# Performance work log

Hardware: AMD Instinct MI355X
Metric: run time of the kernel (lower is better)

## Reference

```python
import jax, jax.numpy as jnp
import numpy as np
from jax import lax

PAD0, PAD1 = 2, 2  # kernel_size=3 -> pad = (3//2+1, (3+1)//2) = (2, 2)


def make_blur_kernel():
    k = jnp.array([1.0, 3.0, 3.0, 1.0], dtype=jnp.float32)
    k2 = k[None, :] * k[:, None]  # [4,4] binomial
    return k2 / jnp.sum(k2)


def setup_inputs() -> dict:
    key = jax.random.key(0)
    x = jax.random.normal(key, (16, 256, 128, 128), dtype=jnp.float32)
    kernel = make_blur_kernel()  # fixed (buffer) 4x4 normalized binomial filter
    return {"x": x, "kernel": kernel}


def reference(x, kernel):
    # upfirdn2d(x, k, up=1, down=1, padding=(2,2)):
    # zero-pad H and W by (2,2) each, depthwise FIR filter with the 4x4 kernel.
    # Kernel is symmetric, so correlation == convolution.
    C = x.shape[1]
    w = jnp.broadcast_to(kernel[None, None, :, :], (C, 1, 4, 4))  # depthwise OIHW
    out = lax.conv_general_dilated(
        x, w,
        window_strides=(1, 1),
        padding=((PAD0, PAD1), (PAD0, PAD1)),
        feature_group_count=C,
        dimension_numbers=("NCHW", "OIHW", "NCHW"),
    )
    # output: [16, 256, 129, 129] (H + pad0 + pad1 - 4 + 1)
    return out
```

## Files before the change

kernel.cpp:

```cpp
#include <hip/hip_runtime.h>


__global__ __launch_bounds__(512) void blur_half3(
    const float* __restrict__ x,
    const float* __restrict__ kern,
    float* __restrict__ out)
{
    __shared__ __align__(16) float lds[69 * 128 + 8 * 264];

    const int tid  = threadIdx.x;
    const int bid  = blockIdx.x;
    const int wk   = ((bid & 7) << 10) | (bid >> 3);
    const int img  = wk >> 1;
    const int s    = wk & 1;
    const int wv   = tid >> 6;
    const int lane = tid & 63;

    const float* __restrict__ xi = x + (size_t)img * (128 * 128);
    float* __restrict__ oi = out + (size_t)img * (129 * 129);

    const int P0 = s ? 0 : 1;
    const int P1 = s ? 32 : 33;
    for (int p = P0 + wv; p <= P1; p += 8) {
        const int row = 64 * s - 2 + 2 * p;
        const float* src = xi + (size_t)row * 128 + (lane << 2);
        const float* dst = &lds[p * 256];
        __builtin_amdgcn_global_load_lds(
            (const __attribute__((address_space(1))) unsigned int*)src,
            (__attribute__((address_space(3))) unsigned int*)dst, 16, 0, 0);
    }
    if (tid < 256) {
        if (s) lds[8448 + tid] = 0.0f;
        else   lds[tid]        = 0.0f;
    } else if (tid < 384) {
        lds[8448 + tid] = 0.0f;
    }

    float w[4][4];
#pragma unroll
    for (int p = 0; p < 4; ++p)
#pragma unroll
        for (int q = 0; q < 4; ++q)
            w[p][q] = kern[4 * p + q];

    __syncthreads();

    const int c  = tid >> 5;
    const int g  = tid & 31;
    const bool lv = (g >= 1);
    const float* const zrow = &lds[68 * 128];
    float* const obuf = &lds[69 * 128 + wv * 264 + (c & 1) * 132];

    float xv[4][8];

#define LLOAD(S, KK) do {                                                    \
        const float* pb_ = &lds[(4 * c + (KK)) * 128 + 4 * g];               \
        const float* pa_ = lv ? (pb_ - 4) : zrow;                            \
        float4 a_ = *(const float4*)pa_;                                     \
        float4 b_ = *(const float4*)pb_;                                     \
        xv[S][0] = a_.x; xv[S][1] = a_.y; xv[S][2] = a_.z; xv[S][3] = a_.w;  \
        xv[S][4] = b_.x; xv[S][5] = b_.y; xv[S][6] = b_.z; xv[S][7] = b_.w;  \
    } while (0)

#define ACCP(S, P) do {                                                      \
        o0 = fmaf(xv[S][0], w[P][0], o0);                                    \
        o1 = fmaf(xv[S][1], w[P][0], o1);                                    \
        o2 = fmaf(xv[S][2], w[P][0], o2);                                    \
        o3 = fmaf(xv[S][3], w[P][0], o3);                                    \
        o0 = fmaf(xv[S][1], w[P][1], o0);                                    \
        o1 = fmaf(xv[S][2], w[P][1], o1);                                    \
        o2 = fmaf(xv[S][3], w[P][1], o2);                                    \
        o3 = fmaf(xv[S][4], w[P][1], o3);                                    \
        o0 = fmaf(xv[S][2], w[P][2], o0);                                    \
        o1 = fmaf(xv[S][3], w[P][2], o1);                                    \
        o2 = fmaf(xv[S][4], w[P][2], o2);                                    \
        o3 = fmaf(xv[S][5], w[P][2], o3);                                    \
        o0 = fmaf(xv[S][3], w[P][3], o0);                                    \
        o1 = fmaf(xv[S][4], w[P][3], o1);                                    \
        o2 = fmaf(xv[S][5], w[P][3], o2);                                    \
        o3 = fmaf(xv[S][6], w[P][3], o3);                                    \
    } while (0)

#define XROW(S, P) do {                                                      \
        e0 = fmaf(xv[S][4], w[P][0], e0);                                    \
        e0 = fmaf(xv[S][5], w[P][1], e0);                                    \
        e0 = fmaf(xv[S][6], w[P][2], e0);                                    \
        e0 = fmaf(xv[S][7], w[P][3], e0);                                    \
        e1 = fmaf(xv[S][5], w[P][0], e1);                                    \
        e1 = fmaf(xv[S][6], w[P][1], e1);                                    \
        e1 = fmaf(xv[S][7], w[P][2], e1);                                    \
        e2 = fmaf(xv[S][6], w[P][0], e2);                                    \
        e2 = fmaf(xv[S][7], w[P][1], e2);                                    \
    } while (0)

#define CS(SA, SB, SC, SD, J) do {                                           \
        float o0 = 0.f, o1 = 0.f, o2 = 0.f, o3 = 0.f;                        \
        ACCP(SA, 0); ACCP(SB, 1); ACCP(SC, 2); ACCP(SD, 3);                  \
        *(float4*)&obuf[4 * g] = make_float4(o0, o1, o2, o3);                \
        if (g == 31) {                                                       \
            float e0 = 0.f, e1 = 0.f, e2 = 0.f;                              \
            XROW(SA, 0); XROW(SB, 1); XROW(SC, 2); XROW(SD, 3);              \
            *(float2*)&obuf[128] = make_float2(e0, e1);    \
            obuf[130] = e2;                                \
        }                                                                    \
        asm volatile("s_waitcnt lgkmcnt(0)" ::: "memory");                   \
        __builtin_amdgcn_sched_barrier(0);                                   \
        {                                                                    \
            float* po_ = oi + (size_t)(64 * s + 4 * c + (J)) * 129;          \
            _Pragma("unroll")                                                \
            for (int k_ = 0; k_ < 4; ++k_)                                   \
                po_[g + 32 * k_] = obuf[2 + g + 32 * k_];                    \
            if (g == 0) po_[128] = obuf[130];                                \
        }                                                                    \
    } while (0)

    {
        LLOAD(0, 0); LLOAD(1, 1); LLOAD(2, 2); LLOAD(3, 3);
        CS(0, 1, 2, 3, 0); LLOAD(0, 4);
        CS(1, 2, 3, 0, 1); LLOAD(1, 5);
        CS(2, 3, 0, 1, 2); LLOAD(2, 6);
        CS(3, 0, 1, 2, 3);
        if (s == 1 && c == 15) {
            LLOAD(3, 7);
            CS(0, 1, 2, 3, 4);
        }
    }

#undef LLOAD
#undef ACCP
#undef XROW
#undef CS
}

extern "C" void kernel_launch(void* const* d_in, const int* in_sizes, int n_in,
                              void* d_out, int out_size, void* d_ws, size_t ws_size,
                              hipStream_t stream) {
    const float* x    = (const float*)d_in[0];
    const float* kern = (const float*)d_in[1];
    float* out        = (float*)d_out;

    dim3 grid(8192), block(512);
    hipLaunchKernelGGL(blur_half3, grid, block, 0, stream, x, kern, out);
}
```

Measured before the change: 109.9 us.

## Replace block barrier with producer-consumer LDS flag pipeline and direct stores

Wave 0 now issues all global-to-LDS row loads and publishes progress through an LDS flag as vmcnt drains, while the other waves spin on the flag and start computing as soon as their rows land. This replaces the full __syncthreads after loading. The LDS staging buffer for output rows is removed, and results are written straight to global memory with unaligned scalar stores. Out-of-range rows are clamped on load and masked to zero when read. The risks are spin-wait overhead, a single wave issuing all the loads, poorer store coalescing, and depending on LDS flag ordering being correct.

```diff
diff --git a/kernel.cpp b/kernel.cpp
--- a/kernel.cpp
+++ b/kernel.cpp
@@ -1,12 +1,12 @@
 #include <hip/hip_runtime.h>
 
 
-__global__ __launch_bounds__(512) void blur_half3(
+__global__ __launch_bounds__(512) void blur_pc(
     const float* __restrict__ x,
     const float* __restrict__ kern,
     float* __restrict__ out)
 {
-    __shared__ __align__(16) float lds[69 * 128 + 8 * 264];
+    __shared__ __align__(16) float lds[68 * 128 + 128 + 4];
 
     const int tid  = threadIdx.x;
     const int bid  = blockIdx.x;
@@ -15,49 +15,64 @@
     const int s    = wk & 1;
     const int wv   = tid >> 6;
     const int lane = tid & 63;
+    const int h    = lane >> 5;
+    const int g    = lane & 31;
+    const bool lv  = (g >= 1);
 
-    const float* __restrict__ xi = x + (size_t)img * (128 * 128);
-    float* __restrict__ oi = out + (size_t)img * (129 * 129);
+    const float* __restrict__ xi = x + (size_t)img * 16384;
+    float* __restrict__ oi = out + (size_t)img * 16641;
 
-    const int P0 = s ? 0 : 1;
-    const int P1 = s ? 32 : 33;
-    for (int p = P0 + wv; p <= P1; p += 8) {
-        const int row = 64 * s - 2 + 2 * p;
-        const float* src = xi + (size_t)row * 128 + (lane << 2);
-        const float* dst = &lds[p * 256];
-        __builtin_amdgcn_global_load_lds(
-            (const __attribute__((address_space(1))) unsigned int*)src,
-            (__attribute__((address_space(3))) unsigned int*)dst, 16, 0, 0);
-    }
-    if (tid < 256) {
-        if (s) lds[8448 + tid] = 0.0f;
-        else   lds[tid]        = 0.0f;
-    } else if (tid < 384) {
-        lds[8448 + tid] = 0.0f;
-    }
+    volatile int* flag = (volatile int*)&lds[68 * 128 + 128];
+    const float* const zrow = &lds[68 * 128];
 
     float w[4][4];
 #pragma unroll
     for (int p = 0; p < 4; ++p)
 #pragma unroll
-        for (int q = 0; q < 4; ++q)
-            w[p][q] = kern[4 * p + q];
+        for (int d = 0; d < 4; ++d)
+            w[p][d] = kern[4 * p + d];
+    __builtin_amdgcn_sched_barrier(0);
 
-    __syncthreads();
+    if (tid < 128) lds[68 * 128 + tid] = 0.0f;
+    if (tid == 0)  *flag = 0;
+    asm volatile("s_waitcnt lgkmcnt(0)" ::: "memory");
+    __builtin_amdgcn_s_barrier();
 
-    const int c  = tid >> 5;
-    const int g  = tid & 31;
-    const bool lv = (g >= 1);
-    const float* const zrow = &lds[68 * 128];
-    float* const obuf = &lds[69 * 128 + wv * 264 + (c & 1) * 132];
+    if (wv == 0) {
+        for (int p = 0; p < 34; ++p) {
+            int row = 64 * s - 2 + 2 * p;
+            row = row < 0 ? 0 : (row > 126 ? 126 : row);
+            const float* src = xi + (size_t)row * 128 + (lane << 2);
+            const float* dst = &lds[p * 256];
+            __builtin_amdgcn_global_load_lds(
+                (const __attribute__((address_space(1))) unsigned int*)src,
+                (__attribute__((address_space(3))) unsigned int*)dst,
+                16, 0, 0);
+        }
+        __builtin_amdgcn_sched_barrier(0);
+#define PUB(NSTR, V) do {                                                    \
+        asm volatile("s_waitcnt vmcnt(" NSTR ")" ::: "memory");              \
+        __builtin_amdgcn_sched_barrier(0);                                   \
+        if (lane == 0) *flag = (V);                                          \
+    } while (0)
+        PUB("28", 6);  PUB("22", 12); PUB("16", 18);
+        PUB("10", 24); PUB("4", 30);  PUB("0", 34);
+#undef PUB
+    }
+
+    const int lbase = (wv == 0) ? 56 : 8 * (wv - 1);
+    const int r0    = lbase + h;
 
     float xv[4][8];
 
-#define LLOAD(S, KK) do {                                                    \
-        const float* pb_ = &lds[(4 * c + (KK)) * 128 + 4 * g];               \
-        const float* pa_ = lv ? (pb_ - 4) : zrow;                            \
+#define LLOAD(S, T) do {                                                     \
+        const int t_ = (T);                                                  \
+        const float* pb_ = &lds[t_ * 128 + 4 * g];                           \
+        const bool okr_ = (unsigned)(64 * s - 2 + t_) < 128u;                \
+        const float* pa_  = (okr_ && lv) ? (pb_ - 4) : zrow;                 \
+        const float* pbv_ = okr_ ? pb_ : zrow;                               \
         float4 a_ = *(const float4*)pa_;                                     \
-        float4 b_ = *(const float4*)pb_;                                     \
+        float4 b_ = *(const float4*)pbv_;                                    \
         xv[S][0] = a_.x; xv[S][1] = a_.y; xv[S][2] = a_.z; xv[S][3] = a_.w;  \
         xv[S][4] = b_.x; xv[S][5] = b_.y; xv[S][6] = b_.z; xv[S][7] = b_.w;  \
     } while (0)
@@ -93,43 +108,54 @@
         e2 = fmaf(xv[S][7], w[P][1], e2);                                    \
     } while (0)
 
-#define CS(SA, SB, SC, SD, J) do {                                           \
+#define CS(SA, SB, SC, SD, LR, EN) do {                                      \
         float o0 = 0.f, o1 = 0.f, o2 = 0.f, o3 = 0.f;                        \
         ACCP(SA, 0); ACCP(SB, 1); ACCP(SC, 2); ACCP(SD, 3);                  \
-        *(float4*)&obuf[4 * g] = make_float4(o0, o1, o2, o3);                \
-        if (g == 31) {                                                       \
-            float e0 = 0.f, e1 = 0.f, e2 = 0.f;                              \
-            XROW(SA, 0); XROW(SB, 1); XROW(SC, 2); XROW(SD, 3);              \
-            *(float2*)&obuf[128] = make_float2(e0, e1);    \
-            obuf[130] = e2;                                \
-        }                                                                    \
-        asm volatile("s_waitcnt lgkmcnt(0)" ::: "memory");                   \
-        __builtin_amdgcn_sched_barrier(0);                                   \
-        {                                                                    \
-            float* po_ = oi + (size_t)(64 * s + 4 * c + (J)) * 129;          \
-            _Pragma("unroll")                                                \
-            for (int k_ = 0; k_ < 4; ++k_)                                   \
-                po_[g + 32 * k_] = obuf[2 + g + 32 * k_];                    \
-            if (g == 0) po_[128] = obuf[130];                                \
+        if (EN) {                                                            \
+            float* po_ = oi + (size_t)(64 * s + (LR)) * 129 + 4 * g - 2;     \
+            if (lv) { po_[0] = o0; po_[1] = o1; }                            \
+            po_[2] = o2;                                                     \
+            po_[3] = o3;                                                     \
+            if (g == 31) {                                                   \
+                float e0 = 0.f, e1 = 0.f, e2 = 0.f;                          \
+                XROW(SA, 0); XROW(SB, 1); XROW(SC, 2); XROW(SD, 3);          \
+                po_[4] = e0; po_[5] = e1; po_[6] = e2;    \
+            }                                                                \
         }                                                                    \
     } while (0)
 
-    {
-        LLOAD(0, 0); LLOAD(1, 1); LLOAD(2, 2); LLOAD(3, 3);
-        CS(0, 1, 2, 3, 0); LLOAD(0, 4);
-        CS(1, 2, 3, 0, 1); LLOAD(1, 5);
-        CS(2, 3, 0, 1, 2); LLOAD(2, 6);
-        CS(3, 0, 1, 2, 3);
-        if (s == 1 && c == 15) {
-            LLOAD(3, 7);
-            CS(0, 1, 2, 3, 4);
-        }
+#define SPIN(NEED) do {                                                      \
+        while (*flag < (NEED)) __builtin_amdgcn_s_sleep(1);                  \
+        asm volatile("" ::: "memory");                                       \
+        __builtin_amdgcn_sched_barrier(0);                                   \
+    } while (0)
+
+    SPIN(lbase / 2 + 3);
+    LLOAD(0, r0 + 0); LLOAD(1, r0 + 1); LLOAD(2, r0 + 2); LLOAD(3, r0 + 3);
+    CS(0, 1, 2, 3, lbase + 0 + h, true);
+
+    SPIN(lbase / 2 + 4);
+    LLOAD(0, r0 + 4); LLOAD(1, r0 + 5);
+    CS(2, 3, 0, 1, lbase + 2 + h, true);
+
+    SPIN(lbase / 2 + 5);
+    LLOAD(2, r0 + 6); LLOAD(3, r0 + 7);
+    CS(0, 1, 2, 3, lbase + 4 + h, true);
+
+    SPIN(lbase / 2 + 6);
+    LLOAD(0, r0 + 8); LLOAD(1, r0 + 9);
+    CS(2, 3, 0, 1, lbase + 6 + h, true);
+
+    if (s == 1 && wv == 0) {
+        LLOAD(0, 64); LLOAD(1, 65); LLOAD(2, 66); LLOAD(3, 67);
+        CS(0, 1, 2, 3, 64, (h == 0));
     }
 
 #undef LLOAD
 #undef ACCP
 #undef XROW
 #undef CS
+#undef SPIN
 }
 
 extern "C" void kernel_launch(void* const* d_in, const int* in_sizes, int n_in,
@@ -140,5 +166,5 @@
     float* out        = (float*)d_out;
 
     dim3 grid(8192), block(512);
-    hipLaunchKernelGGL(blur_half3, grid, block, 0, stream, x, kern, out);
+    hipLaunchKernelGGL(blur_pc, grid, block, 0, stream, x, kern, out);
 }
```

Result: slower. 117.8 us (+7.2%).
